# Optimization experiments

Measured on AMD Instinct MI355X. Metric: run time of the kernel, lower is better.

The kernel has to match this reference:

```python
import jax, jax.numpy as jnp
import numpy as np

N, E, IN_F, EDGE_F, HID, S = 200000, 600000, 28, 4, 128, 20000
NUM_LAYERS = 4
L = NUM_LAYERS - 1
BN_EPS = 1e-5


def setup_inputs() -> dict:
    key = jax.random.key(0)
    ks = jax.random.split(key, 20)
    p = lambda k, shape: (jax.random.normal(k, shape, dtype=jnp.float32) * 0.1)
    return {
        'x': jax.random.normal(ks[0], (N, IN_F), dtype=jnp.float32),
        'edge_index': jax.random.randint(ks[1], (2, E), 0, N),
        'edge_attr': jax.random.normal(ks[2], (E, EDGE_F), dtype=jnp.float32),
        'edge_weight': jax.random.uniform(ks[3], (E,), dtype=jnp.float32),
        'node_mask': (jax.random.uniform(ks[4], (N,)) > 0.5).astype(jnp.float32),
        'subgraphs2nodes': jax.random.randint(ks[5], (N,), 0, S),
        # layer-1 params (in_features -> hidden)
        'be1_W1': p(ks[6], (EDGE_F, IN_F)), 'be1_b1': jnp.zeros((IN_F,), jnp.float32),
        'be1_W2': p(ks[7], (IN_F, IN_F)), 'be1_b2': jnp.zeros((IN_F,), jnp.float32),
        'm1_W1': p(ks[8], (IN_F, HID)), 'm1_b1': jnp.zeros((HID,), jnp.float32),
        'm1_W2': p(ks[9], (HID, HID)), 'm1_b2': jnp.zeros((HID,), jnp.float32),
        'bn1_g': jnp.ones((HID,), jnp.float32), 'bn1_b': jnp.zeros((HID,), jnp.float32),
        'eps1': jnp.zeros((), jnp.float32),
        # layers 2..NUM_LAYERS, stacked (hidden -> hidden)
        'beW1': p(ks[10], (L, EDGE_F, HID)), 'beb1': jnp.zeros((L, HID), jnp.float32),
        'beW2': p(ks[11], (L, HID, HID)), 'beb2': jnp.zeros((L, HID), jnp.float32),
        'mW1': p(ks[12], (L, HID, HID)), 'mb1': jnp.zeros((L, HID), jnp.float32),
        'mW2': p(ks[13], (L, HID, HID)), 'mb2': jnp.zeros((L, HID), jnp.float32),
        'bng': jnp.ones((L, HID), jnp.float32), 'bnb': jnp.zeros((L, HID), jnp.float32),
        'eps': jnp.zeros((L,), jnp.float32),
    }


def _mlp2(h, W1, b1, W2, b2):
    # Linear -> ReLU -> Linear
    return jnp.dot(jax.nn.relu(jnp.dot(h, W1) + b1), W2) + b2


def _gine(x, src, dst, edge_attr, edge_weight, eps,
          beW1, beb1, beW2, beb2, W1, b1, W2, b2, g, beta):
    # bond encoder on edge features
    e = _mlp2(edge_attr, beW1, beb1, beW2, beb2)            # [E, d]
    # message: relu(x_j + e_ij) * w_ij, aggregated at dst via scatter-add
    m = jax.nn.relu(x[src] + e) * edge_weight[:, None]      # [E, d]
    aggr = jax.ops.segment_sum(m, dst, num_segments=N)      # [N, d]
    h = (1.0 + eps) * x + aggr
    # node MLP: Linear,ReLU,Linear,BN(train mode),ReLU
    h = _mlp2(h, W1, b1, W2, b2)
    mu = jnp.mean(h, axis=0)
    var = jnp.mean((h - mu) ** 2, axis=0)
    h = (h - mu) * jax.lax.rsqrt(var + BN_EPS) * g + beta
    return jax.nn.relu(h)


def reference(x, edge_index, edge_attr, edge_weight, node_mask, subgraphs2nodes,
              be1_W1, be1_b1, be1_W2, be1_b2, m1_W1, m1_b1, m1_W2, m1_b2,
              bn1_g, bn1_b, eps1,
              beW1, beb1, beW2, beb2, mW1, mb1, mW2, mb2, bng, bnb, eps):
    src, dst = edge_index[0], edge_index[1]
    h = _gine(x, src, dst, edge_attr, edge_weight, eps1,
              be1_W1, be1_b1, be1_W2, be1_b2,
              m1_W1, m1_b1, m1_W2, m1_b2, bn1_g, bn1_b)
    for i in range(L):
        h_new = _gine(h, src, dst, edge_attr, edge_weight, eps[i],
                      beW1[i], beb1[i], beW2[i], beb2[i],
                      mW1[i], mb1[i], mW2[i], mb2[i], bng[i], bnb[i])
        h = h + h_new  # residual
    # float node_mask branch + global_add_pool over subgraphs2nodes
    h = h * node_mask[:, None]
    return jax.ops.segment_sum(h, subgraphs2nodes, num_segments=S)  # [S, HID]
```

## Files before the change

### kernel.cpp

```cpp
#include <hip/hip_runtime.h>
#include <hip/hip_bf16.h>


#define BNEPS 1e-5f
#define LDA 136
#define SCAN_NB 240

typedef __attribute__((ext_vector_type(8))) short bf16x8;
typedef __attribute__((ext_vector_type(8))) unsigned short u16x8;
typedef __attribute__((ext_vector_type(4))) float f32x4;

__device__ inline short f2bf(float f) {
    __hip_bfloat16 h = __float2bfloat16(f);
    return *reinterpret_cast<short*>(&h);
}
__device__ inline unsigned short f2bfu(float f) {
    __hip_bfloat16 h = __float2bfloat16(f);
    return *reinterpret_cast<unsigned short*>(&h);
}
__device__ inline float bf2f(unsigned short u) {
    union { unsigned int i; float f; } v; v.i = ((unsigned int)u) << 16; return v.f;
}

__global__ __launch_bounds__(256) void k_prep(
    const float* __restrict__ m1W2, const float* __restrict__ beW2,
    const float* __restrict__ mW1, const float* __restrict__ mW2,
    short* __restrict__ out)
{
    __shared__ float tileS[64][65];
    int b = blockIdx.x, mat = b >> 2, t = b & 3;
    const float* Wsrc;
    if (mat == 0) Wsrc = m1W2;
    else {
        int l = (mat - 1) / 3, which = (mat - 1) % 3;
        Wsrc = (which == 0) ? beW2 + (size_t)l * 16384
             : (which == 1) ? mW1 + (size_t)l * 16384
             :                mW2 + (size_t)l * 16384;
    }
    short* dst = out + (size_t)mat * 16384;
    int tr = (t >> 1) * 64, tc = (t & 1) * 64;
    for (int i = threadIdx.x; i < 4096; i += 256) {
        int r = i >> 6, c = i & 63;
        tileS[r][c] = Wsrc[(size_t)(tr + r) * 128 + (tc + c)];
    }
    __syncthreads();
    for (int i = threadIdx.x; i < 4096; i += 256) {
        int n = i >> 6, k = i & 63;
        dst[(size_t)(tc + n) * 128 + (tr + k)] = f2bf(tileS[k][n]);
    }
}

__global__ __launch_bounds__(256) void k_prep1(
    const float* __restrict__ W1, short* __restrict__ out)
{
    for (int i = threadIdx.x; i < 128 * 32; i += 256) {
        int n = i >> 5, k = i & 31;
        out[i] = (k < 28) ? f2bf(W1[(size_t)k * 128 + n]) : (short)0;
    }
}

__global__ __launch_bounds__(256) void k_prep28(
    const float* __restrict__ W2, short* __restrict__ out)
{
    for (int i = threadIdx.x; i < 32 * 32; i += 256) {
        int n = i >> 5, k = i & 31;
        out[i] = (n < 28 && k < 28) ? f2bf(W2[(size_t)k * 28 + n]) : (short)0;
    }
}

__global__ __launch_bounds__(256) void k_prepx(
    const float* __restrict__ x, unsigned short* __restrict__ xbf, int N)
{
    int total = N * 32;
    for (int i = blockIdx.x * 256 + threadIdx.x; i < total; i += gridDim.x * 256) {
        int n = i >> 5, c = i & 31;
        xbf[i] = (c < 28) ? f2bfu(x[(size_t)n * 28 + c]) : (unsigned short)0;
    }
}

__global__ __launch_bounds__(256) void k_count(
    const int* __restrict__ ei, int* __restrict__ counts, int E)
{
    for (int e = blockIdx.x * 256 + threadIdx.x; e < E; e += gridDim.x * 256)
        atomicAdd(&counts[ei[E + e]], 1);
}

__global__ __launch_bounds__(256) void k_count2(
    const int* __restrict__ s2n, const float* __restrict__ mask,
    int* __restrict__ counts2, int N)
{
    for (int n = blockIdx.x * 256 + threadIdx.x; n < N; n += gridDim.x * 256)
        if (mask[n] != 0.f) atomicAdd(&counts2[s2n[n]], 1);
}

__global__ __launch_bounds__(256) void k_scanA(
    const int* __restrict__ counts, int* __restrict__ bsum, int N, int seg)
{
    __shared__ int red[256];
    int b = blockIdx.x;
    int lo = b * seg, hi = min(lo + seg, N);
    int s = 0;
    for (int i = lo + threadIdx.x; i < hi; i += 256) s += counts[i];
    red[threadIdx.x] = s;
    __syncthreads();
    for (int d = 128; d > 0; d >>= 1) {
        if (threadIdx.x < d) red[threadIdx.x] += red[threadIdx.x + d];
        __syncthreads();
    }
    if (threadIdx.x == 0) bsum[b] = red[0];
}

__global__ __launch_bounds__(256) void k_scanB(
    int* __restrict__ bsum, int nb, int* __restrict__ offs, int N)
{
    __shared__ int sh[256];
    int v = (threadIdx.x < nb) ? bsum[threadIdx.x] : 0;
    sh[threadIdx.x] = v;
    __syncthreads();
    for (int d = 1; d < 256; d <<= 1) {
        int t = (threadIdx.x >= d) ? sh[threadIdx.x - d] : 0;
        __syncthreads();
        sh[threadIdx.x] += t;
        __syncthreads();
    }
    if (threadIdx.x < nb) bsum[threadIdx.x] = sh[threadIdx.x] - v;
    if (threadIdx.x == 0) offs[N] = sh[255];
}

__global__ __launch_bounds__(256) void k_scanC(
    const int* __restrict__ counts, const int* __restrict__ bsum,
    int* __restrict__ offs, int* __restrict__ cursor, int N, int seg)
{
    __shared__ int sh[256];
    int b = blockIdx.x;
    int lo = b * seg, hi = min(lo + seg, N);
    int base = bsum[b];
    for (int t0 = lo; t0 < hi; t0 += 256) {
        int i = t0 + threadIdx.x;
        int v = (i < hi) ? counts[i] : 0;
        sh[threadIdx.x] = v;
        __syncthreads();
        for (int d = 1; d < 256; d <<= 1) {
            int t = (threadIdx.x >= d) ? sh[threadIdx.x - d] : 0;
            __syncthreads();
            sh[threadIdx.x] += t;
            __syncthreads();
        }
        int excl = base + sh[threadIdx.x] - v;
        if (i < hi) { offs[i] = excl; cursor[i] = excl; }
        int tileTotal = sh[255];
        __syncthreads();
        base += tileTotal;
    }
}

__global__ __launch_bounds__(256) void k_scatter(
    const int* __restrict__ ei, const float* __restrict__ ew,
    const float4* __restrict__ ea4,
    int* __restrict__ cursor, int2* __restrict__ pmeta,
    float4* __restrict__ pea4, int E)
{
    for (int e = blockIdx.x * 256 + threadIdx.x; e < E; e += gridDim.x * 256) {
        int d = ei[E + e];
        int pos = atomicAdd(&cursor[d], 1);
        pmeta[pos] = make_int2(ei[e], __float_as_int(ew[e]));
        pea4[pos] = ea4[e];
    }
}

__global__ __launch_bounds__(256) void k_scatter2(
    const int* __restrict__ s2n, const float* __restrict__ mask,
    int* __restrict__ cursor2, int* __restrict__ perm2, int N)
{
    for (int n = blockIdx.x * 256 + threadIdx.x; n < N; n += gridDim.x * 256)
        if (mask[n] != 0.f) {
            int pos = atomicAdd(&cursor2[s2n[n]], 1);
            perm2[pos] = n;
        }
}

__global__ __launch_bounds__(256) void k_emsg(
    const float4* __restrict__ pea4,
    const float* __restrict__ W1, const float* __restrict__ b1,
    const short* __restrict__ W2t, const float* __restrict__ b2,
    unsigned short* __restrict__ emsg, const int* __restrict__ offs,
    int n0, int n1)
{
    __shared__ short Bs[128 * LDA];
    __shared__ short As[64 * LDA];
    __shared__ float eas[64][4];
    int e0 = offs[n0], e1 = offs[n1];
    int tid = threadIdx.x;
    for (int i = tid; i < 2048; i += 256) {
        int n = (i * 8) >> 7, k = (i * 8) & 127;
        *(bf16x8*)&Bs[n * LDA + k] = *(const bf16x8*)&W2t[i * 8];
    }
    int j = tid & 127, half = tid >> 7;
    float w10 = W1[j], w11 = W1[128 + j], w12 = W1[256 + j], w13 = W1[384 + j];
    float b1j = b1[j];
    int w = tid >> 6, lane = tid & 63;
    int l15 = lane & 15, quad = lane >> 4;
    __syncthreads();

    int numTiles = (e1 - e0 + 63) >> 6;
    for (int tile = blockIdx.x; tile < numTiles; tile += gridDim.x) {
        int base = e0 + tile * 64;
        __syncthreads();
        if (tid < 64) {
            int k = base + tid;
            float4 a = make_float4(0.f, 0.f, 0.f, 0.f);
            if (k < e1) a = pea4[k];
            eas[tid][0] = a.x; eas[tid][1] = a.y; eas[tid][2] = a.z; eas[tid][3] = a.w;
        }
        __syncthreads();
        #pragma unroll
        for (int q = 0; q < 32; ++q) {
            int e = half * 32 + q;
            float t = fmaf(eas[e][0], w10, fmaf(eas[e][1], w11,
                      fmaf(eas[e][2], w12, fmaf(eas[e][3], w13, b1j))));
            As[e * LDA + j] = f2bf(fmaxf(t, 0.f));
        }
        __syncthreads();
        f32x4 acc[8];
        #pragma unroll
        for (int nt = 0; nt < 8; ++nt) acc[nt] = (f32x4){0.f, 0.f, 0.f, 0.f};
        #pragma unroll
        for (int kt = 0; kt < 4; ++kt) {
            bf16x8 af = *(bf16x8*)&As[(w * 16 + l15) * LDA + kt * 32 + quad * 8];
            #pragma unroll
            for (int nt = 0; nt < 8; ++nt) {
                bf16x8 bf = *(bf16x8*)&Bs[(nt * 16 + l15) * LDA + kt * 32 + quad * 8];
                acc[nt] = __builtin_amdgcn_mfma_f32_16x16x32_bf16(af, bf, acc[nt], 0, 0, 0);
            }
        }
        #pragma unroll
        for (int nt = 0; nt < 8; ++nt) {
            int col = nt * 16 + l15;
            float b2c = b2[col];
            #pragma unroll
            for (int r = 0; r < 4; ++r) {
                int row = w * 16 + quad * 4 + r;
                As[row * LDA + col] = f2bf(acc[nt][r] + b2c);
            }
        }
        __syncthreads();
        #pragma unroll
        for (int kk = 0; kk < 4; ++kk) {
            int i = tid + kk * 256;
            int row = (i * 8) >> 7, col = (i * 8) & 127;
            int gr = base + row;
            if (gr < e1)
                *(bf16x8*)&emsg[(size_t)(gr - e0) * 128 + col] = *(bf16x8*)&As[row * LDA + col];
        }
    }
}

__global__ __launch_bounds__(256) void k_emsg28_mm(
    const float4* __restrict__ pea4,
    const float* __restrict__ W1, const float* __restrict__ b1,
    const short* __restrict__ W2t28,
    const float* __restrict__ b2,
    unsigned short* __restrict__ emsg28, int E)
{
    __shared__ short Bs[32 * 40];
    __shared__ short As[64 * 40];
    __shared__ float eas[64][4];
    __shared__ float b2s[32];
    int tid = threadIdx.x;
    for (int i = tid; i < 32 * 32; i += 256) {
        int n = i >> 5, k = i & 31;
        Bs[n * 40 + k] = W2t28[i];
    }
    if (tid < 32) b2s[tid] = (tid < 28) ? b2[tid] : 0.f;
    int j = tid & 31, sub = tid >> 5;
    float w10 = 0.f, w11 = 0.f, w12 = 0.f, w13 = 0.f, b1j = 0.f;
    if (j < 28) { w10 = W1[j]; w11 = W1[28 + j]; w12 = W1[56 + j]; w13 = W1[84 + j]; b1j = b1[j]; }
    int w = tid >> 6, lane = tid & 63;
    int l15 = lane & 15, quad = lane >> 4;
    __syncthreads();

    int numTiles = (E + 63) >> 6;
    for (int tile = blockIdx.x; tile < numTiles; tile += gridDim.x) {
        int base = tile * 64;
        __syncthreads();
        if (tid < 64) {
            int k = base + tid;
            float4 a = (k < E) ? pea4[k] : make_float4(0.f, 0.f, 0.f, 0.f);
            eas[tid][0] = a.x; eas[tid][1] = a.y; eas[tid][2] = a.z; eas[tid][3] = a.w;
        }
        __syncthreads();
        #pragma unroll
        for (int q = 0; q < 8; ++q) {
            int e = q * 8 + sub;
            float t = fmaf(eas[e][0], w10, fmaf(eas[e][1], w11,
                      fmaf(eas[e][2], w12, fmaf(eas[e][3], w13, b1j))));
            As[e * 40 + j] = (j < 28) ? f2bf(fmaxf(t, 0.f)) : (short)0;
        }
        __syncthreads();
        f32x4 acc[2];
        acc[0] = (f32x4){0.f, 0.f, 0.f, 0.f};
        acc[1] = (f32x4){0.f, 0.f, 0.f, 0.f};
        bf16x8 af = *(bf16x8*)&As[(w * 16 + l15) * 40 + quad * 8];
        #pragma unroll
        for (int nt = 0; nt < 2; ++nt) {
            bf16x8 bf = *(bf16x8*)&Bs[(nt * 16 + l15) * 40 + quad * 8];
            acc[nt] = __builtin_amdgcn_mfma_f32_16x16x32_bf16(af, bf, acc[nt], 0, 0, 0);
        }
        __syncthreads();
        #pragma unroll
        for (int nt = 0; nt < 2; ++nt) {
            int col = nt * 16 + l15;
            float bb = b2s[col];
            #pragma unroll
            for (int r = 0; r < 4; ++r)
                As[(w * 16 + quad * 4 + r) * 40 + col] = f2bf(acc[nt][r] + bb);
        }
        __syncthreads();
        for (int i = tid; i < 64 * 28; i += 256) {
            int row = i / 28, col = i - row * 28;
            int gr = base + row;
            if (gr < E) emsg28[(size_t)gr * 28 + col] = As[row * 40 + col];
        }
    }
}

__global__ __launch_bounds__(256) void k_gather(
    const unsigned short* __restrict__ h, const int* __restrict__ offs,
    const int2* __restrict__ pmeta, const unsigned short* __restrict__ emsg,
    unsigned short* __restrict__ a0,
    const float* __restrict__ epsp, int epsIdx,
    int n0, int n1)
{
    int grp = threadIdx.x >> 5, lane = threadIdx.x & 31;
    int n = n0 + blockIdx.x * 8 + grp;
    if (n >= n1) return;
    int e0 = offs[n0];
    int k0 = offs[n], k1 = offs[n + 1];
    float s = 1.0f + epsp[epsIdx];
    ushort4 hv0 = *(const ushort4*)&h[(size_t)n * 128 + lane * 4];
    float m0 = s * bf2f(hv0.x), m1 = s * bf2f(hv0.y);
    float m2 = s * bf2f(hv0.z), m3 = s * bf2f(hv0.w);
    for (int k = k0; k < k1; ++k) {
        int2 mt = pmeta[k];
        float w = __int_as_float(mt.y);
        ushort4 ev = *(const ushort4*)&emsg[(size_t)(k - e0) * 128 + lane * 4];
        ushort4 hv = *(const ushort4*)&h[(size_t)mt.x * 128 + lane * 4];
        m0 += fmaxf(bf2f(hv.x) + bf2f(ev.x), 0.f) * w;
        m1 += fmaxf(bf2f(hv.y) + bf2f(ev.y), 0.f) * w;
        m2 += fmaxf(bf2f(hv.z) + bf2f(ev.z), 0.f) * w;
        m3 += fmaxf(bf2f(hv.w) + bf2f(ev.w), 0.f) * w;
    }
    ushort4 o;
    o.x = f2bfu(m0); o.y = f2bfu(m1); o.z = f2bfu(m2); o.w = f2bfu(m3);
    *(ushort4*)&a0[(size_t)n * 128 + lane * 4] = o;
}

__global__ __launch_bounds__(256) void k_gather28(
    const float* __restrict__ x, const unsigned short* __restrict__ xbf,
    const int* __restrict__ offs,
    const int2* __restrict__ pmeta, const unsigned short* __restrict__ emsg28,
    const float* __restrict__ eps1, float* __restrict__ u28, int N)
{
    int grp = threadIdx.x >> 5, lane = threadIdx.x & 31;
    int n = blockIdx.x * 8 + grp;
    if (n >= N || lane >= 28) return;
    float s = 1.0f + eps1[0];
    int k0 = offs[n], k1 = offs[n + 1];
    float m = 0.f;
    for (int k = k0; k < k1; ++k) {
        int2 mt = pmeta[k];
        float w = __int_as_float(mt.y);
        float e = bf2f(emsg28[(size_t)k * 28 + lane]);
        float xs = bf2f(xbf[(size_t)mt.x * 32 + lane]);
        m += fmaxf(xs + e, 0.f) * w;
    }
    u28[(size_t)n * 28 + lane] = fmaf(s, x[(size_t)n * 28 + lane], m);
}

__global__ __launch_bounds__(512) void k_mlp(
    const unsigned short* __restrict__ src, const short* __restrict__ Wt1,
    const float* __restrict__ b1, const short* __restrict__ Wt2,
    const float* __restrict__ b2, unsigned short* __restrict__ dst,
    float* __restrict__ stats, int N)
{
    __shared__ short Bs1[128 * LDA];
    __shared__ short Bs2[128 * LDA];
    __shared__ short As[128 * LDA];
    __shared__ float sstat[256];
    int tid = threadIdx.x;
    for (int i = tid; i < 2048; i += 512) {
        int n = (i * 8) >> 7, k = (i * 8) & 127;
        *(bf16x8*)&Bs1[n * LDA + k] = *(const bf16x8*)&Wt1[i * 8];
        *(bf16x8*)&Bs2[n * LDA + k] = *(const bf16x8*)&Wt2[i * 8];
    }
    if (tid < 256) sstat[tid] = 0.f;
    int w = tid >> 6, lane = tid & 63;
    int l15 = lane & 15, quad = lane >> 4;
    float b1r[8], b2r[8], lsum[8], lsq[8];
    #pragma unroll
    for (int nt = 0; nt < 8; ++nt) {
        int col = nt * 16 + l15;
        b1r[nt] = b1[col]; b2r[nt] = b2[col];
        lsum[nt] = 0.f; lsq[nt] = 0.f;
    }
    __syncthreads();

    int numTiles = (N + 127) >> 7;
    for (int tile = blockIdx.x; tile < numTiles; tile += gridDim.x) {
        int base = tile * 128;
        __syncthreads();
        #pragma unroll
        for (int kk = 0; kk < 4; ++kk) {
            int i = tid + kk * 512;
            int row = (i * 8) >> 7, col = (i * 8) & 127;
            int rr = base + row;
            bf16x8 v;
            if (rr < N) v = *(const bf16x8*)&src[(size_t)rr * 128 + col];
            else        v = (bf16x8){0,0,0,0,0,0,0,0};
            *(bf16x8*)&As[row * LDA + col] = v;
        }
        __syncthreads();
        f32x4 acc[8];
        #pragma unroll
        for (int nt = 0; nt < 8; ++nt) acc[nt] = (f32x4){0.f, 0.f, 0.f, 0.f};
        #pragma unroll
        for (int kt = 0; kt < 4; ++kt) {
            bf16x8 af = *(bf16x8*)&As[(w * 16 + l15) * LDA + kt * 32 + quad * 8];
            #pragma unroll
            for (int nt = 0; nt < 8; ++nt) {
                bf16x8 bf = *(bf16x8*)&Bs1[(nt * 16 + l15) * LDA + kt * 32 + quad * 8];
                acc[nt] = __builtin_amdgcn_mfma_f32_16x16x32_bf16(af, bf, acc[nt], 0, 0, 0);
            }
        }
        #pragma unroll
        for (int nt = 0; nt < 8; ++nt) {
            int col = nt * 16 + l15;
            #pragma unroll
            for (int r = 0; r < 4; ++r)
                As[(w * 16 + quad * 4 + r) * LDA + col] = f2bf(fmaxf(acc[nt][r] + b1r[nt], 0.f));
        }
        __syncthreads();
        #pragma unroll
        for (int nt = 0; nt < 8; ++nt) acc[nt] = (f32x4){0.f, 0.f, 0.f, 0.f};
        #pragma unroll
        for (int kt = 0; kt < 4; ++kt) {
            bf16x8 af = *(bf16x8*)&As[(w * 16 + l15) * LDA + kt * 32 + quad * 8];
            #pragma unroll
            for (int nt = 0; nt < 8; ++nt) {
                bf16x8 bf = *(bf16x8*)&Bs2[(nt * 16 + l15) * LDA + kt * 32 + quad * 8];
                acc[nt] = __builtin_amdgcn_mfma_f32_16x16x32_bf16(af, bf, acc[nt], 0, 0, 0);
            }
        }
        int row0 = base + w * 16 + quad * 4;
        #pragma unroll
        for (int nt = 0; nt < 8; ++nt) {
            int col = nt * 16 + l15;
            #pragma unroll
            for (int r = 0; r < 4; ++r) {
                float z = acc[nt][r] + b2r[nt];
                if (row0 + r < N) { lsum[nt] += z; lsq[nt] = fmaf(z, z, lsq[nt]); }
                As[(w * 16 + quad * 4 + r) * LDA + col] = f2bf(z);
            }
        }
        __syncthreads();
        #pragma unroll
        for (int kk = 0; kk < 4; ++kk) {
            int i = tid + kk * 512;
            int row = (i * 8) >> 7, col = (i * 8) & 127;
            int rr = base + row;
            if (rr < N)
                *(bf16x8*)&dst[(size_t)rr * 128 + col] = *(bf16x8*)&As[row * LDA + col];
        }
    }
    #pragma unroll
    for (int nt = 0; nt < 8; ++nt) {
        int col = nt * 16 + l15;
        atomicAdd(&sstat[col], lsum[nt]);
        atomicAdd(&sstat[128 + col], lsq[nt]);
    }
    __syncthreads();
    if (tid < 256) atomicAdd(&stats[tid], sstat[tid]);
}

__global__ __launch_bounds__(512) void k_mlp1(
    const float* __restrict__ u28, const short* __restrict__ Wt1p,
    const float* __restrict__ b1, const short* __restrict__ Wt2,
    const float* __restrict__ b2, unsigned short* __restrict__ dst,
    float* __restrict__ stats, int N)
{
    __shared__ short Bs1[128 * 40];
    __shared__ short Bs2[128 * LDA];
    __shared__ short As[128 * LDA];
    __shared__ short A28[128 * 40];
    __shared__ float sstat[256];
    int tid = threadIdx.x;
    for (int i = tid; i < 128 * 32; i += 512) {
        int n = i >> 5, k = i & 31;
        Bs1[n * 40 + k] = Wt1p[i];
    }
    for (int i = tid; i < 2048; i += 512) {
        int n = (i * 8) >> 7, k = (i * 8) & 127;
        *(bf16x8*)&Bs2[n * LDA + k] = *(const bf16x8*)&Wt2[i * 8];
    }
    {
        int r = tid >> 2, c = tid & 3;
        if (tid < 512) A28[r * 40 + 28 + c] = 0;
    }
    if (tid < 256) sstat[tid] = 0.f;
    int w = tid >> 6, lane = tid & 63;
    int l15 = lane & 15, quad = lane >> 4;
    float b1r[8], b2r[8], lsum[8], lsq[8];
    #pragma unroll
    for (int nt = 0; nt < 8; ++nt) {
        int col = nt * 16 + l15;
        b1r[nt] = b1[col]; b2r[nt] = b2[col];
        lsum[nt] = 0.f; lsq[nt] = 0.f;
    }
    __syncthreads();

    int numTiles = (N + 127) >> 7;
    for (int tile = blockIdx.x; tile < numTiles; tile += gridDim.x) {
        int base = tile * 128;
        __syncthreads();
        for (int i = tid; i < 128 * 28; i += 512) {
            int row = i / 28, col = i - row * 28;
            int rr = base + row;
            A28[row * 40 + col] = (rr < N) ? f2bf(u28[(size_t)rr * 28 + col]) : (short)0;
        }
        __syncthreads();
        f32x4 acc[8];
        #pragma unroll
        for (int nt = 0; nt < 8; ++nt) acc[nt] = (f32x4){0.f, 0.f, 0.f, 0.f};
        {
            bf16x8 af = *(bf16x8*)&A28[(w * 16 + l15) * 40 + quad * 8];
            #pragma unroll
            for (int nt = 0; nt < 8; ++nt) {
                bf16x8 bf = *(bf16x8*)&Bs1[(nt * 16 + l15) * 40 + quad * 8];
                acc[nt] = __builtin_amdgcn_mfma_f32_16x16x32_bf16(af, bf, acc[nt], 0, 0, 0);
            }
        }
        #pragma unroll
        for (int nt = 0; nt < 8; ++nt) {
            int col = nt * 16 + l15;
            #pragma unroll
            for (int r = 0; r < 4; ++r)
                As[(w * 16 + quad * 4 + r) * LDA + col] = f2bf(fmaxf(acc[nt][r] + b1r[nt], 0.f));
        }
        __syncthreads();
        #pragma unroll
        for (int nt = 0; nt < 8; ++nt) acc[nt] = (f32x4){0.f, 0.f, 0.f, 0.f};
        #pragma unroll
        for (int kt = 0; kt < 4; ++kt) {
            bf16x8 af = *(bf16x8*)&As[(w * 16 + l15) * LDA + kt * 32 + quad * 8];
            #pragma unroll
            for (int nt = 0; nt < 8; ++nt) {
                bf16x8 bf = *(bf16x8*)&Bs2[(nt * 16 + l15) * LDA + kt * 32 + quad * 8];
                acc[nt] = __builtin_amdgcn_mfma_f32_16x16x32_bf16(af, bf, acc[nt], 0, 0, 0);
            }
        }
        int row0 = base + w * 16 + quad * 4;
        #pragma unroll
        for (int nt = 0; nt < 8; ++nt) {
            int col = nt * 16 + l15;
            #pragma unroll
            for (int r = 0; r < 4; ++r) {
                float z = acc[nt][r] + b2r[nt];
                if (row0 + r < N) { lsum[nt] += z; lsq[nt] = fmaf(z, z, lsq[nt]); }
                As[(w * 16 + quad * 4 + r) * LDA + col] = f2bf(z);
            }
        }
        __syncthreads();
        #pragma unroll
        for (int kk = 0; kk < 4; ++kk) {
            int i = tid + kk * 512;
            int row = (i * 8) >> 7, col = (i * 8) & 127;
            int rr = base + row;
            if (rr < N)
                *(bf16x8*)&dst[(size_t)rr * 128 + col] = *(bf16x8*)&As[row * LDA + col];
        }
    }
    #pragma unroll
    for (int nt = 0; nt < 8; ++nt) {
        int col = nt * 16 + l15;
        atomicAdd(&sstat[col], lsum[nt]);
        atomicAdd(&sstat[128 + col], lsq[nt]);
    }
    __syncthreads();
    if (tid < 256) atomicAdd(&stats[tid], sstat[tid]);
}

__global__ __launch_bounds__(128) void k_stats(
    const float* __restrict__ stats, const float* __restrict__ g,
    const float* __restrict__ b, float* __restrict__ ss, float invN)
{
    int j = threadIdx.x;
    float mu  = stats[j] * invN;
    float var = fmaf(stats[128 + j], invN, -mu * mu);
    float sc  = rsqrtf(fmaxf(var, 0.f) + BNEPS) * g[j];
    ss[j] = sc;
    ss[128 + j] = fmaf(-mu, sc, b[j]);
}

__global__ __launch_bounds__(256) void k_bn(
    const unsigned short* __restrict__ z, const float* __restrict__ ss,
    unsigned short* __restrict__ h, int residual, int N)
{
    int idx8 = blockIdx.x * 256 + threadIdx.x;
    int stride = gridDim.x * 256;
    int c0 = (idx8 & 15) * 8;
    float scl[8], sht[8];
    #pragma unroll
    for (int r = 0; r < 8; ++r) { scl[r] = ss[c0 + r]; sht[r] = ss[128 + c0 + r]; }
    int total8 = N * 16;
    for (; idx8 < total8; idx8 += stride) {
        int n = idx8 >> 4;
        u16x8 z8 = *(const u16x8*)&z[(size_t)n * 128 + c0];
        float hn[8];
        #pragma unroll
        for (int r = 0; r < 8; ++r)
            hn[r] = fmaxf(fmaf(bf2f(z8[r]), scl[r], sht[r]), 0.f);
        if (residual) {
            u16x8 h8 = *(const u16x8*)&h[(size_t)n * 128 + c0];
            #pragma unroll
            for (int r = 0; r < 8; ++r) hn[r] += bf2f(h8[r]);
        }
        u16x8 o;
        #pragma unroll
        for (int r = 0; r < 8; ++r) o[r] = f2bfu(hn[r]);
        *(u16x8*)&h[(size_t)n * 128 + c0] = o;
    }
}

__global__ __launch_bounds__(256) void k_poolbn(
    const unsigned short* __restrict__ z, const unsigned short* __restrict__ hprev,
    const float* __restrict__ ss, const int* __restrict__ offs2,
    const int* __restrict__ perm2, float* __restrict__ out, int S)
{
    int w = threadIdx.x >> 6, lane = threadIdx.x & 63;
    int s = blockIdx.x * 4 + w;
    if (s >= S) return;
    int c0 = lane * 2;
    float scl0 = ss[c0], scl1 = ss[c0 + 1];
    float sht0 = ss[128 + c0], sht1 = ss[128 + c0 + 1];
    int k0 = offs2[s], k1 = offs2[s + 1];
    float a0 = 0.f, a1 = 0.f;
    for (int k = k0; k < k1; ++k) {
        int n = perm2[k];
        ushort2 zv = *(const ushort2*)&z[(size_t)n * 128 + c0];
        ushort2 hv = *(const ushort2*)&hprev[(size_t)n * 128 + c0];
        a0 += fmaxf(fmaf(bf2f(zv.x), scl0, sht0), 0.f) + bf2f(hv.x);
        a1 += fmaxf(fmaf(bf2f(zv.y), scl1, sht1), 0.f) + bf2f(hv.y);
    }
    *(float2*)&out[(size_t)s * 128 + c0] = make_float2(a0, a1);
}

extern "C" void kernel_launch(void* const* d_in, const int* in_sizes, int n_in,
                              void* d_out, int out_size, void* d_ws, size_t ws_size,
                              hipStream_t stream) {
    const float* x    = (const float*)d_in[0];
    const int*   ei   = (const int*)d_in[1];
    const float* ea   = (const float*)d_in[2];
    const float* ew   = (const float*)d_in[3];
    const float* mask = (const float*)d_in[4];
    const int*   s2n  = (const int*)d_in[5];
    const float* be1W1 = (const float*)d_in[6];
    const float* be1b1 = (const float*)d_in[7];
    const float* be1W2 = (const float*)d_in[8];
    const float* be1b2 = (const float*)d_in[9];
    const float* m1W1  = (const float*)d_in[10];
    const float* m1b1  = (const float*)d_in[11];
    const float* m1W2  = (const float*)d_in[12];
    const float* m1b2  = (const float*)d_in[13];
    const float* bn1g  = (const float*)d_in[14];
    const float* bn1b  = (const float*)d_in[15];
    const float* eps1  = (const float*)d_in[16];
    const float* beW1  = (const float*)d_in[17];
    const float* beb1  = (const float*)d_in[18];
    const float* beW2  = (const float*)d_in[19];
    const float* beb2  = (const float*)d_in[20];
    const float* mW1   = (const float*)d_in[21];
    const float* mb1   = (const float*)d_in[22];
    const float* mW2   = (const float*)d_in[23];
    const float* mb2   = (const float*)d_in[24];
    const float* bng   = (const float*)d_in[25];
    const float* bnb   = (const float*)d_in[26];
    const float* epsL  = (const float*)d_in[27];

    const int N = in_sizes[0] / 28;
    const int E = in_sizes[1] / 2;
    const int S = out_size / 128;
    const float invN = 1.0f / (float)N;
    const int NS = N / 2;
    const int EMC = E / 2 + 8192;

    auto al16 = [](size_t v) { return (v + 15) & ~(size_t)15; };
    char* ws = (char*)d_ws;
    size_t offH      = 0;
    size_t offA0     = al16(offH + (size_t)N * 256);
    size_t offEm     = al16(offA0 + (size_t)N * 256);
    size_t emBytes   = (size_t)EMC * 256;
    if ((size_t)E * 56 > emBytes) emBytes = (size_t)E * 56;
    size_t offStats  = al16(offEm + emBytes);
    size_t offSS     = al16(offStats + 4096);
    size_t offWts    = al16(offSS + 1024);
    size_t offCounts = al16(offWts + 10 * 16384 * 2 + 4096 * 2 + 1024 * 2);
    size_t offOffs   = al16(offCounts + (size_t)N * 4);
    size_t offCursor = al16(offOffs + (size_t)(N + 1) * 4);
    size_t offPmeta  = al16(offCursor + (size_t)N * 4);
    size_t offPea    = al16(offPmeta + (size_t)E * 8);
    size_t offBsum   = al16(offPea + (size_t)E * 16);
    size_t offCnt2   = al16(offBsum + SCAN_NB * 4);
    size_t offOffs2  = al16(offCnt2 + (size_t)S * 4);
    size_t offCur2   = al16(offOffs2 + (size_t)(S + 1) * 4);
    size_t offPerm2  = al16(offCur2 + (size_t)S * 4);
    size_t need      = offPerm2 + (size_t)N * 4;
    if (ws_size < need) return;

    unsigned short* h    = (unsigned short*)(ws + offH);
    unsigned short* a0   = (unsigned short*)(ws + offA0);
    unsigned short* emsg = (unsigned short*)(ws + offEm);
    float* u28    = (float*)(ws + offA0);
    unsigned short* xbf = (unsigned short*)(ws + offA0 + 26214400);
    float* stats  = (float*)(ws + offStats);
    float* ssbuf  = (float*)(ws + offSS);
    short* wts    = (short*)(ws + offWts);
    short* w1p    = wts + 10 * 16384;
    short* w2p28  = w1p + 4096;
    int*   counts = (int*)(ws + offCounts);
    int*   offs   = (int*)(ws + offOffs);
    int*   cursor = (int*)(ws + offCursor);
    int2*  pmeta  = (int2*)(ws + offPmeta);
    float4* pea4  = (float4*)(ws + offPea);
    int*   bsum   = (int*)(ws + offBsum);
    int*   cnt2   = (int*)(ws + offCnt2);
    int*   offs2  = (int*)(ws + offOffs2);
    int*   cur2   = (int*)(ws + offCur2);
    int*   perm2  = (int*)(ws + offPerm2);
    const float4* ea4 = (const float4*)ea;

    hipMemsetAsync(stats, 0, 4 * 256 * sizeof(float), stream);
    hipMemsetAsync(counts, 0, (size_t)N * sizeof(int), stream);
    hipMemsetAsync(cnt2, 0, (size_t)S * sizeof(int), stream);

    k_prep<<<40, 256, 0, stream>>>(m1W2, beW2, mW1, mW2, wts);
    k_prep1<<<1, 256, 0, stream>>>(m1W1, w1p);
    k_prep28<<<1, 256, 0, stream>>>(be1W2, w2p28);
    k_prepx<<<512, 256, 0, stream>>>(x, xbf, N);

    const int seg = (N + SCAN_NB - 1) / SCAN_NB;
    k_count<<<1024, 256, 0, stream>>>(ei, counts, E);
    k_scanA<<<SCAN_NB, 256, 0, stream>>>(counts, bsum, N, seg);
    k_scanB<<<1, 256, 0, stream>>>(bsum, SCAN_NB, offs, N);
    k_scanC<<<SCAN_NB, 256, 0, stream>>>(counts, bsum, offs, cursor, N, seg);
    k_scatter<<<1024, 256, 0, stream>>>(ei, ew, ea4, cursor, pmeta, pea4, E);

    const int seg2 = (S + SCAN_NB - 1) / SCAN_NB;
    k_count2<<<512, 256, 0, stream>>>(s2n, mask, cnt2, N);
    k_scanA<<<SCAN_NB, 256, 0, stream>>>(cnt2, bsum, S, seg2);
    k_scanB<<<1, 256, 0, stream>>>(bsum, SCAN_NB, offs2, S);
    k_scanC<<<SCAN_NB, 256, 0, stream>>>(cnt2, bsum, offs2, cur2, S, seg2);
    k_scatter2<<<512, 256, 0, stream>>>(s2n, mask, cur2, perm2, N);

    auto wt_be = [&](int l) { return wts + (size_t)(1 + 3 * l + 0) * 16384; };
    auto wt_m1 = [&](int l) { return wts + (size_t)(1 + 3 * l + 1) * 16384; };
    auto wt_m2 = [&](int l) { return wts + (size_t)(1 + 3 * l + 2) * 16384; };

    k_emsg28_mm<<<2048, 256, 0, stream>>>(pea4, be1W1, be1b1, w2p28, be1b2, emsg, E);
    k_gather28<<<(N + 7) / 8, 256, 0, stream>>>(x, xbf, offs, pmeta, emsg, eps1, u28, N);
    k_mlp1<<<256, 512, 0, stream>>>(u28, w1p, m1b1, wts , m1b2, h, stats, N);
    k_stats<<<1, 128, 0, stream>>>(stats, bn1g, bn1b, ssbuf, invN);
    k_bn<<<2048, 256, 0, stream>>>(h, ssbuf, h, 0, N);

    for (int l = 0; l < 3; ++l) {
        for (int c = 0; c < 2; ++c) {
            int n0 = (c == 0) ? 0 : NS;
            int n1 = (c == 0) ? NS : N;
            k_emsg<<<2048, 256, 0, stream>>>(pea4,
                beW1 + (size_t)l * 512, beb1 + (size_t)l * 128,
                wt_be(l), beb2 + (size_t)l * 128, emsg, offs, n0, n1);
            k_gather<<<(n1 - n0 + 7) / 8, 256, 0, stream>>>(h, offs, pmeta, emsg, a0,
                epsL, l, n0, n1);
        }
        k_mlp<<<256, 512, 0, stream>>>(a0, wt_m1(l), mb1 + (size_t)l * 128,
                                       wt_m2(l), mb2 + (size_t)l * 128, a0,
                                       stats + 256 * (l + 1), N);
        k_stats<<<1, 128, 0, stream>>>(stats + 256 * (l + 1),
            bng + (size_t)l * 128, bnb + (size_t)l * 128, ssbuf, invN);
        if (l < 2) {
            k_bn<<<2048, 256, 0, stream>>>(a0, ssbuf, h, 1, N);
        }
    }

    k_poolbn<<<(S + 3) / 4, 256, 0, stream>>>(a0, h, ssbuf, offs2, perm2,
                                              (float*)d_out, S);
}
```

Baseline: 1.052 ms.

## Hold MLP weight fragments in registers and retile warps to 32x64 blocks

The fused node-MLP kernels change their warp tiling. Each of the 8 waves used to own 16 rows across all 128 columns; now it owns 32 rows across 64 columns. Each wave loads its B-operand weight fragments from shared memory into registers once, before the tile loop, so the per-tile weight LDS reads go away and each A fragment feeds 4 MFMAs. The grid for k_mlp and k_mlp1 doubles to 512 blocks. In exchange, the kernels need many more VGPRs for the cached fragments, which could lower occupancy or spill, and add extra barriers because waves now write rows that other waves read.

```diff
diff --git a/kernel.cpp b/kernel.cpp
--- a/kernel.cpp
+++ b/kernel.cpp
@@ -396,14 +396,27 @@
     if (tid < 256) sstat[tid] = 0.f;
     int w = tid >> 6, lane = tid & 63;
     int l15 = lane & 15, quad = lane >> 4;
-    float b1r[8], b2r[8], lsum[8], lsq[8];
+    int cg = w >> 2;
+    int rb = (w & 3) * 32;
+    __syncthreads();
+
+    bf16x8 B1f[4][4], B2f[4][4];
+    float b1r[4], b2r[4];
     #pragma unroll
-    for (int nt = 0; nt < 8; ++nt) {
-        int col = nt * 16 + l15;
+    for (int nt = 0; nt < 4; ++nt) {
+        int col = cg * 64 + nt * 16 + l15;
         b1r[nt] = b1[col]; b2r[nt] = b2[col];
-        lsum[nt] = 0.f; lsq[nt] = 0.f;
-    }
-    __syncthreads();
+        #pragma unroll
+        for (int kt = 0; kt < 4; ++kt) {
+            B1f[nt][kt] = *(bf16x8*)&Bs1[col * LDA + kt * 32 + quad * 8];
+            B2f[nt][kt] = *(bf16x8*)&Bs2[col * LDA + kt * 32 + quad * 8];
+        }
+    }
+    float lsum[2][4], lsq[2][4];
+    #pragma unroll
+    for (int rg = 0; rg < 2; ++rg)
+        #pragma unroll
+        for (int nt = 0; nt < 4; ++nt) { lsum[rg][nt] = 0.f; lsq[rg][nt] = 0.f; }
 
     int numTiles = (N + 127) >> 7;
     for (int tile = blockIdx.x; tile < numTiles; tile += gridDim.x) {
@@ -420,48 +433,61 @@
             *(bf16x8*)&As[row * LDA + col] = v;
         }
         __syncthreads();
-        f32x4 acc[8];
-        #pragma unroll
-        for (int nt = 0; nt < 8; ++nt) acc[nt] = (f32x4){0.f, 0.f, 0.f, 0.f};
-        #pragma unroll
-        for (int kt = 0; kt < 4; ++kt) {
-            bf16x8 af = *(bf16x8*)&As[(w * 16 + l15) * LDA + kt * 32 + quad * 8];
-            #pragma unroll
-            for (int nt = 0; nt < 8; ++nt) {
-                bf16x8 bf = *(bf16x8*)&Bs1[(nt * 16 + l15) * LDA + kt * 32 + quad * 8];
-                acc[nt] = __builtin_amdgcn_mfma_f32_16x16x32_bf16(af, bf, acc[nt], 0, 0, 0);
+        f32x4 acc[2][4];
+        #pragma unroll
+        for (int rg = 0; rg < 2; ++rg)
+            #pragma unroll
+            for (int nt = 0; nt < 4; ++nt) acc[rg][nt] = (f32x4){0.f, 0.f, 0.f, 0.f};
+        #pragma unroll
+        for (int rg = 0; rg < 2; ++rg) {
+            #pragma unroll
+            for (int kt = 0; kt < 4; ++kt) {
+                bf16x8 af = *(bf16x8*)&As[(rb + rg * 16 + l15) * LDA + kt * 32 + quad * 8];
+                #pragma unroll
+                for (int nt = 0; nt < 4; ++nt)
+                    acc[rg][nt] = __builtin_amdgcn_mfma_f32_16x16x32_bf16(af, B1f[nt][kt], acc[rg][nt], 0, 0, 0);
             }
         }
-        #pragma unroll
-        for (int nt = 0; nt < 8; ++nt) {
-            int col = nt * 16 + l15;
-            #pragma unroll
-            for (int r = 0; r < 4; ++r)
-                As[(w * 16 + quad * 4 + r) * LDA + col] = f2bf(fmaxf(acc[nt][r] + b1r[nt], 0.f));
-        }
-        __syncthreads();
-        #pragma unroll
-        for (int nt = 0; nt < 8; ++nt) acc[nt] = (f32x4){0.f, 0.f, 0.f, 0.f};
-        #pragma unroll
-        for (int kt = 0; kt < 4; ++kt) {
-            bf16x8 af = *(bf16x8*)&As[(w * 16 + l15) * LDA + kt * 32 + quad * 8];
-            #pragma unroll
-            for (int nt = 0; nt < 8; ++nt) {
-                bf16x8 bf = *(bf16x8*)&Bs2[(nt * 16 + l15) * LDA + kt * 32 + quad * 8];
-                acc[nt] = __builtin_amdgcn_mfma_f32_16x16x32_bf16(af, bf, acc[nt], 0, 0, 0);
+        __syncthreads();
+        #pragma unroll
+        for (int rg = 0; rg < 2; ++rg)
+            #pragma unroll
+            for (int nt = 0; nt < 4; ++nt) {
+                int col = cg * 64 + nt * 16 + l15;
+                #pragma unroll
+                for (int r = 0; r < 4; ++r)
+                    As[(rb + rg * 16 + quad * 4 + r) * LDA + col] =
+                        f2bf(fmaxf(acc[rg][nt][r] + b1r[nt], 0.f));
             }
-        }
-        int row0 = base + w * 16 + quad * 4;
-        #pragma unroll
-        for (int nt = 0; nt < 8; ++nt) {
-            int col = nt * 16 + l15;
-            #pragma unroll
-            for (int r = 0; r < 4; ++r) {
-                float z = acc[nt][r] + b2r[nt];
-                if (row0 + r < N) { lsum[nt] += z; lsq[nt] = fmaf(z, z, lsq[nt]); }
-                As[(w * 16 + quad * 4 + r) * LDA + col] = f2bf(z);
+        __syncthreads();
+        #pragma unroll
+        for (int rg = 0; rg < 2; ++rg)
+            #pragma unroll
+            for (int nt = 0; nt < 4; ++nt) acc[rg][nt] = (f32x4){0.f, 0.f, 0.f, 0.f};
+        #pragma unroll
+        for (int rg = 0; rg < 2; ++rg) {
+            #pragma unroll
+            for (int kt = 0; kt < 4; ++kt) {
+                bf16x8 af = *(bf16x8*)&As[(rb + rg * 16 + l15) * LDA + kt * 32 + quad * 8];
+                #pragma unroll
+                for (int nt = 0; nt < 4; ++nt)
+                    acc[rg][nt] = __builtin_amdgcn_mfma_f32_16x16x32_bf16(af, B2f[nt][kt], acc[rg][nt], 0, 0, 0);
             }
         }
+        __syncthreads();
+        #pragma unroll
+        for (int rg = 0; rg < 2; ++rg)
+            #pragma unroll
+            for (int nt = 0; nt < 4; ++nt) {
+                int col = cg * 64 + nt * 16 + l15;
+                int row0 = base + rb + rg * 16 + quad * 4;
+                #pragma unroll
+                for (int r = 0; r < 4; ++r) {
+                    float z = acc[rg][nt][r] + b2r[nt];
+                    if (row0 + r < N) { lsum[rg][nt] += z; lsq[rg][nt] = fmaf(z, z, lsq[rg][nt]); }
+                    As[(rb + rg * 16 + quad * 4 + r) * LDA + col] = f2bf(z);
+                }
+            }
         __syncthreads();
         #pragma unroll
         for (int kk = 0; kk < 4; ++kk) {
@@ -473,10 +499,10 @@
         }
     }
     #pragma unroll
-    for (int nt = 0; nt < 8; ++nt) {
-        int col = nt * 16 + l15;
-        atomicAdd(&sstat[col], lsum[nt]);
-        atomicAdd(&sstat[128 + col], lsq[nt]);
+    for (int nt = 0; nt < 4; ++nt) {
+        int col = cg * 64 + nt * 16 + l15;
+        atomicAdd(&sstat[col], lsum[0][nt] + lsum[1][nt]);
+        atomicAdd(&sstat[128 + col], lsq[0][nt] + lsq[1][nt]);
     }
     __syncthreads();
     if (tid < 256) atomicAdd(&stats[tid], sstat[tid]);
@@ -504,19 +530,30 @@
     }
     {
         int r = tid >> 2, c = tid & 3;
-        if (tid < 512) A28[r * 40 + 28 + c] = 0;
+        if (r < 128) A28[r * 40 + 28 + c] = 0;
     }
     if (tid < 256) sstat[tid] = 0.f;
     int w = tid >> 6, lane = tid & 63;
     int l15 = lane & 15, quad = lane >> 4;
-    float b1r[8], b2r[8], lsum[8], lsq[8];
+    int cg = w >> 2, rb = (w & 3) * 32;
+    __syncthreads();
+
+    bf16x8 B1f[4], B2f[4][4];
+    float b1r[4], b2r[4];
     #pragma unroll
-    for (int nt = 0; nt < 8; ++nt) {
-        int col = nt * 16 + l15;
+    for (int nt = 0; nt < 4; ++nt) {
+        int col = cg * 64 + nt * 16 + l15;
         b1r[nt] = b1[col]; b2r[nt] = b2[col];
-        lsum[nt] = 0.f; lsq[nt] = 0.f;
-    }
-    __syncthreads();
+        B1f[nt] = *(bf16x8*)&Bs1[col * 40 + quad * 8];
+        #pragma unroll
+        for (int kt = 0; kt < 4; ++kt)
+            B2f[nt][kt] = *(bf16x8*)&Bs2[col * LDA + kt * 32 + quad * 8];
+    }
+    float lsum[2][4], lsq[2][4];
+    #pragma unroll
+    for (int rg = 0; rg < 2; ++rg)
+        #pragma unroll
+        for (int nt = 0; nt < 4; ++nt) { lsum[rg][nt] = 0.f; lsq[rg][nt] = 0.f; }
 
     int numTiles = (N + 127) >> 7;
     for (int tile = blockIdx.x; tile < numTiles; tile += gridDim.x) {
@@ -528,47 +565,57 @@
             A28[row * 40 + col] = (rr < N) ? f2bf(u28[(size_t)rr * 28 + col]) : (short)0;
         }
         __syncthreads();
-        f32x4 acc[8];
-        #pragma unroll
-        for (int nt = 0; nt < 8; ++nt) acc[nt] = (f32x4){0.f, 0.f, 0.f, 0.f};
-        {
-            bf16x8 af = *(bf16x8*)&A28[(w * 16 + l15) * 40 + quad * 8];
-            #pragma unroll
-            for (int nt = 0; nt < 8; ++nt) {
-                bf16x8 bf = *(bf16x8*)&Bs1[(nt * 16 + l15) * 40 + quad * 8];
-                acc[nt] = __builtin_amdgcn_mfma_f32_16x16x32_bf16(af, bf, acc[nt], 0, 0, 0);
+        f32x4 acc[2][4];
+        #pragma unroll
+        for (int rg = 0; rg < 2; ++rg)
+            #pragma unroll
+            for (int nt = 0; nt < 4; ++nt) acc[rg][nt] = (f32x4){0.f, 0.f, 0.f, 0.f};
+        #pragma unroll
+        for (int rg = 0; rg < 2; ++rg) {
+            bf16x8 af = *(bf16x8*)&A28[(rb + rg * 16 + l15) * 40 + quad * 8];
+            #pragma unroll
+            for (int nt = 0; nt < 4; ++nt)
+                acc[rg][nt] = __builtin_amdgcn_mfma_f32_16x16x32_bf16(af, B1f[nt], acc[rg][nt], 0, 0, 0);
+        }
+        #pragma unroll
+        for (int rg = 0; rg < 2; ++rg)
+            #pragma unroll
+            for (int nt = 0; nt < 4; ++nt) {
+                int col = cg * 64 + nt * 16 + l15;
+                #pragma unroll
+                for (int r = 0; r < 4; ++r)
+                    As[(rb + rg * 16 + quad * 4 + r) * LDA + col] =
+                        f2bf(fmaxf(acc[rg][nt][r] + b1r[nt], 0.f));
             }
-        }
-        #pragma unroll
-        for (int nt = 0; nt < 8; ++nt) {
-            int col = nt * 16 + l15;
-            #pragma unroll
-            for (int r = 0; r < 4; ++r)
-                As[(w * 16 + quad * 4 + r) * LDA + col] = f2bf(fmaxf(acc[nt][r] + b1r[nt], 0.f));
-        }
-        __syncthreads();
-        #pragma unroll
-        for (int nt = 0; nt < 8; ++nt) acc[nt] = (f32x4){0.f, 0.f, 0.f, 0.f};
-        #pragma unroll
-        for (int kt = 0; kt < 4; ++kt) {
-            bf16x8 af = *(bf16x8*)&As[(w * 16 + l15) * LDA + kt * 32 + quad * 8];
-            #pragma unroll
-            for (int nt = 0; nt < 8; ++nt) {
-                bf16x8 bf = *(bf16x8*)&Bs2[(nt * 16 + l15) * LDA + kt * 32 + quad * 8];
-                acc[nt] = __builtin_amdgcn_mfma_f32_16x16x32_bf16(af, bf, acc[nt], 0, 0, 0);
+        __syncthreads();
+        #pragma unroll
+        for (int rg = 0; rg < 2; ++rg)
+            #pragma unroll
+            for (int nt = 0; nt < 4; ++nt) acc[rg][nt] = (f32x4){0.f, 0.f, 0.f, 0.f};
+        #pragma unroll
+        for (int rg = 0; rg < 2; ++rg) {
+            #pragma unroll
+            for (int kt = 0; kt < 4; ++kt) {
+                bf16x8 af = *(bf16x8*)&As[(rb + rg * 16 + l15) * LDA + kt * 32 + quad * 8];
+                #pragma unroll
+                for (int nt = 0; nt < 4; ++nt)
+                    acc[rg][nt] = __builtin_amdgcn_mfma_f32_16x16x32_bf16(af, B2f[nt][kt], acc[rg][nt], 0, 0, 0);
             }
         }
-        int row0 = base + w * 16 + quad * 4;
-        #pragma unroll
-        for (int nt = 0; nt < 8; ++nt) {
-            int col = nt * 16 + l15;
-            #pragma unroll
-            for (int r = 0; r < 4; ++r) {
-                float z = acc[nt][r] + b2r[nt];
-                if (row0 + r < N) { lsum[nt] += z; lsq[nt] = fmaf(z, z, lsq[nt]); }
-                As[(w * 16 + quad * 4 + r) * LDA + col] = f2bf(z);
+        __syncthreads();
+        #pragma unroll
+        for (int rg = 0; rg < 2; ++rg)
+            #pragma unroll
+            for (int nt = 0; nt < 4; ++nt) {
+                int col = cg * 64 + nt * 16 + l15;
+                int row0 = base + rb + rg * 16 + quad * 4;
+                #pragma unroll
+                for (int r = 0; r < 4; ++r) {
+                    float z = acc[rg][nt][r] + b2r[nt];
+                    if (row0 + r < N) { lsum[rg][nt] += z; lsq[rg][nt] = fmaf(z, z, lsq[rg][nt]); }
+                    As[(rb + rg * 16 + quad * 4 + r) * LDA + col] = f2bf(z);
+                }
             }
-        }
         __syncthreads();
         #pragma unroll
         for (int kk = 0; kk < 4; ++kk) {
@@ -580,10 +627,10 @@
         }
     }
     #pragma unroll
-    for (int nt = 0; nt < 8; ++nt) {
-        int col = nt * 16 + l15;
-        atomicAdd(&sstat[col], lsum[nt]);
-        atomicAdd(&sstat[128 + col], lsq[nt]);
+    for (int nt = 0; nt < 4; ++nt) {
+        int col = cg * 64 + nt * 16 + l15;
+        atomicAdd(&sstat[col], lsum[0][nt] + lsum[1][nt]);
+        atomicAdd(&sstat[128 + col], lsq[0][nt] + lsq[1][nt]);
     }
     __syncthreads();
     if (tid < 256) atomicAdd(&stats[tid], sstat[tid]);
@@ -767,7 +814,7 @@
 
     k_emsg28_mm<<<2048, 256, 0, stream>>>(pea4, be1W1, be1b1, w2p28, be1b2, emsg, E);
     k_gather28<<<(N + 7) / 8, 256, 0, stream>>>(x, xbf, offs, pmeta, emsg, eps1, u28, N);
-    k_mlp1<<<256, 512, 0, stream>>>(u28, w1p, m1b1, wts , m1b2, h, stats, N);
+    k_mlp1<<<512, 512, 0, stream>>>(u28, w1p, m1b1, wts , m1b2, h, stats, N);
     k_stats<<<1, 128, 0, stream>>>(stats, bn1g, bn1b, ssbuf, invN);
     k_bn<<<2048, 256, 0, stream>>>(h, ssbuf, h, 0, N);
 
@@ -781,7 +828,7 @@
             k_gather<<<(n1 - n0 + 7) / 8, 256, 0, stream>>>(h, offs, pmeta, emsg, a0,
                 epsL, l, n0, n1);
         }
-        k_mlp<<<256, 512, 0, stream>>>(a0, wt_m1(l), mb1 + (size_t)l * 128,
+        k_mlp<<<512, 512, 0, stream>>>(a0, wt_m1(l), mb1 + (size_t)l * 128,
                                        wt_m2(l), mb2 + (size_t)l * 128, a0,
                                        stats + 256 * (l + 1), N);
         k_stats<<<1, 128, 0, stream>>>(stats + 256 * (l + 1),
```

New measurement: 1.036 ms. No clear change (-1.5%).
